# Performance work log

Hardware: AMD Instinct MI355X
Metric: run time of the kernel (lower is better)

Reference implementation:

```python
import jax, jax.numpy as jnp
import numpy as np

N_NODES = 50000
N_EDGES = 1600000
IN_C, HID_C, OUT_C = 1433, 128, 47


def setup_inputs() -> dict:
    key = jax.random.key(0)
    ks = jax.random.split(key, 5)
    x = jax.random.normal(ks[0], (N_NODES, IN_C), dtype=jnp.float32)
    edge_index = jax.random.randint(ks[1], (2, N_EDGES), 0, N_NODES, dtype=jnp.int32)
    # Glorot-ish init scaled by fan-in
    W1 = jax.random.normal(ks[2], (IN_C, HID_C), dtype=jnp.float32) / np.sqrt(IN_C)
    W2 = jax.random.normal(ks[3], (HID_C, HID_C), dtype=jnp.float32) / np.sqrt(HID_C)
    W3 = jax.random.normal(ks[4], (HID_C, OUT_C), dtype=jnp.float32) / np.sqrt(HID_C)
    b1 = jnp.zeros((HID_C,), jnp.float32)
    b2 = jnp.zeros((HID_C,), jnp.float32)
    b3 = jnp.zeros((OUT_C,), jnp.float32)
    return {"x": x, "edge_index": edge_index, "W1": W1, "b1": b1,
            "W2": W2, "b2": b2, "W3": W3, "b3": b3}


def _gcn_norm(edge_index, n_nodes, dtype):
    # PyG GCNConv default: add self-loops, symmetric D^-1/2 A D^-1/2 norm.
    loops = jnp.arange(n_nodes, dtype=edge_index.dtype)
    src = jnp.concatenate([edge_index[0], loops])
    dst = jnp.concatenate([edge_index[1], loops])
    deg = jax.ops.segment_sum(jnp.ones(src.shape[0], dtype), dst, num_segments=n_nodes)
    dinv = jax.lax.rsqrt(jnp.maximum(deg, 1.0))  # deg >= 1 due to self-loops
    norm = dinv[src] * dinv[dst]  # [E + N]
    return src, dst, norm


def _gcn_layer(h, W, b, src, dst, norm, n_nodes):
    hw = h @ W                       # [N, C_out] dense transform first (cheaper)
    msg = hw[src] * norm[:, None]    # gather + per-edge scale
    out = jax.ops.segment_sum(msg, dst, num_segments=n_nodes)  # scatter-add
    return out + b


def reference(x, edge_index, W1, b1, W2, b2, W3, b3):
    n = x.shape[0]
    src, dst, norm = _gcn_norm(edge_index, n, x.dtype)
    h = jax.nn.relu(_gcn_layer(x, W1, b1, src, dst, norm, n))
    # dropout is identity in eval mode (training=False)
    h = jax.nn.relu(_gcn_layer(h, W2, b2, src, dst, norm, n))
    return _gcn_layer(h, W3, b3, src, dst, norm, n)
```

## Files before the change

kernel.cpp:

```cpp
#include <hip/hip_runtime.h>
#include <math.h>
#include <stdint.h>

#define N_NODES 50000
#define N_EDGES 1600000
#define IN_C    1433
#define HID_C   128
#define OUT_C   47
#define KPAD1   1440

typedef unsigned short u16;

__device__ inline u16 f2bf(float x, float& hf) {
    unsigned u = __float_as_uint(x);
    unsigned r = (u + 0x7FFFu + ((u >> 16) & 1u)) & 0xFFFF0000u;
    hf = __uint_as_float(r);
    return (u16)(r >> 16);
}

__device__ inline void gld_lds16(const void* g, const void* lds) {
    __builtin_amdgcn_global_load_lds(
        (const __attribute__((address_space(1))) unsigned int*)(unsigned long long)(uintptr_t)g,
        (__attribute__((address_space(3))) unsigned int*)(unsigned long long)(unsigned)(uintptr_t)lds,
        16, 0, 0);
}

__global__ __launch_bounds__(256) void k_zero_i(int* p, int n) {
    int i = blockIdx.x * 256 + threadIdx.x;
    if (i < n) p[i] = 0;
}

__global__ __launch_bounds__(256) void k_count(const int* __restrict__ dst, int* __restrict__ cnt) {
    int e = blockIdx.x * 256 + threadIdx.x;
    if (e < N_EDGES) atomicAdd(&cnt[dst[e]], 1);
}

__global__ __launch_bounds__(256) void k_dinv(const int* __restrict__ cnt, float* __restrict__ dinv) {
    int i = blockIdx.x * 256 + threadIdx.x;
    if (i < N_NODES) dinv[i] = rsqrtf(1.0f + (float)cnt[i]);
}

__global__ __launch_bounds__(1024) void k_scan(const int* __restrict__ cnt, int* __restrict__ row_start) {
    __shared__ int sums[1024];
    const int t = threadIdx.x;
    const int CH = (N_NODES + 1023) / 1024;
    const int base = t * CH;
    int s = 0;
    for (int j = 0; j < CH; ++j) { int idx = base + j; if (idx < N_NODES) s += cnt[idx]; }
    sums[t] = s;
    __syncthreads();
    for (int off = 1; off < 1024; off <<= 1) {
        int v = (t >= off) ? sums[t - off] : 0;
        __syncthreads();
        sums[t] += v;
        __syncthreads();
    }
    int run = (t == 0) ? 0 : sums[t - 1];
    for (int j = 0; j < CH; ++j) {
        int idx = base + j;
        if (idx < N_NODES) { row_start[idx] = run; run += cnt[idx]; }
    }
    if (t == 1023) row_start[N_NODES] = N_EDGES;
}

__global__ __launch_bounds__(256) void k_fill(
    const int* __restrict__ src, const int* __restrict__ dst,
    const int* __restrict__ row_start, int* __restrict__ cursor,
    int* __restrict__ csr_src)
{
    int e = blockIdx.x * 256 + threadIdx.x;
    if (e >= N_EDGES) return;
    int t = dst[e];
    int pos = row_start[t] + atomicAdd(&cursor[t], 1);
    csr_src[pos] = src[e];
}

__global__ __launch_bounds__(256) void k_wsplit(
    const float* __restrict__ W, int K, int Kpad,
    u16* __restrict__ Thi, u16* __restrict__ Tlo)
{
    int id = blockIdx.x * 256 + threadIdx.x;
    if (id >= 128 * Kpad) return;
    int n = id / Kpad, k = id - n * Kpad;
    float v = (k < K) ? W[(long)k * HID_C + n] : 0.f;
    float hf; u16 h = f2bf(v, hf);
    float d;  u16 l = f2bf(v - hf, d);
    Thi[id] = h; Tlo[id] = l;
}

template<bool RELU_A>
__global__ __launch_bounds__(256) void k_gemm_mfma(
    const float* __restrict__ A, const u16* __restrict__ BThi,
    const u16* __restrict__ BTlo, float* __restrict__ C,
    int M, int K, int Kpad, int lda)
{
    using bf16x8 = __attribute__((ext_vector_type(8))) short;
    using f32x4  = __attribute__((ext_vector_type(4))) float;

    __shared__ float Af[2][2048];
    __shared__ u16  Bhs[2][4096];
    __shared__ u16  Bls[2][4096];

    const int tid  = threadIdx.x;
    const int wave = tid >> 6, lane = tid & 63;
    const int lr   = lane & 15, quad = lane >> 4;
    const int wm   = (wave >> 1) * 32, wn = (wave & 1) * 64;
    const int m0   = blockIdx.x * 64;

    f32x4 acc[2][4];
#pragma unroll
    for (int i = 0; i < 2; ++i)
#pragma unroll
        for (int j = 0; j < 4; ++j)
#pragma unroll
            for (int r = 0; r < 4; ++r) acc[i][j][r] = 0.f;

    const int nk = (K + 31) >> 5;

    auto stageB = [&](int t, int buf) {
        const int k0 = t * 32;
#pragma unroll
        for (int i = 0; i < 2; ++i) {
            const int gc  = wave * 128 + i * 64;
            const int g   = gc + lane;
            const int row = g >> 2, c = g & 3;
            const int q   = c ^ ((row >> 1) & 3);
            const long goff = (long)row * Kpad + k0 + q * 8;
            gld_lds16(BThi + goff, &Bhs[buf][gc * 8]);
            gld_lds16(BTlo + goff, &Bls[buf][gc * 8]);
        }
    };
    auto stageA = [&](int t, int buf) {
        const int k0 = t * 32;
        if (k0 + 32 <= K) {
#pragma unroll
            for (int i = 0; i < 2; ++i) {
                const int gc  = wave * 128 + i * 64;
                const int g   = gc + lane;
                const int row = g >> 3, c = g & 7;
                const int q   = c ^ (row & 7);
                int gm = m0 + row; if (gm >= M) gm = M - 1;
                gld_lds16(A + (long)gm * lda + k0 + q * 4, &Af[buf][gc * 4]);
            }
        } else {
#pragma unroll
            for (int i = 0; i < 2; ++i) {
                const int g   = wave * 128 + i * 64 + lane;
                const int row = g >> 3, c = g & 7;
                const int q   = c ^ (row & 7);
                int gm = m0 + row; if (gm >= M) gm = M - 1;
                const float* p = A + (long)gm * lda;
                const int kb = k0 + q * 4;
                float4 v;
                v.x = (kb + 0 < K) ? p[kb + 0] : 0.f;
                v.y = (kb + 1 < K) ? p[kb + 1] : 0.f;
                v.z = (kb + 2 < K) ? p[kb + 2] : 0.f;
                v.w = (kb + 3 < K) ? p[kb + 3] : 0.f;
                *(float4*)&Af[buf][g * 4] = v;
            }
        }
    };

    stageA(0, 0); stageB(0, 0);
    __syncthreads();

    for (int t = 0; t < nk; ++t) {
        const int buf = t & 1;
        if (t + 1 < nk) { stageA(t + 1, buf ^ 1); stageB(t + 1, buf ^ 1); }

        bf16x8 ah[2], al[2];
#pragma unroll
        for (int i = 0; i < 2; ++i) {
            const int row = wm + i * 16 + lr;
            const int rx  = row & 7;
            f32x4 x0 = *(const f32x4*)&Af[buf][row * 32 + (((2 * quad)     ^ rx) * 4)];
            f32x4 x1 = *(const f32x4*)&Af[buf][row * 32 + (((2 * quad + 1) ^ rx) * 4)];
            float a8[8] = {x0[0], x0[1], x0[2], x0[3], x1[0], x1[1], x1[2], x1[3]};
#pragma unroll
            for (int c = 0; c < 8; ++c) {
                float x = RELU_A ? fmaxf(a8[c], 0.f) : a8[c];
                float hf; u16 h = f2bf(x, hf);
                float d;  u16 l = f2bf(x - hf, d);
                ah[i][c] = (short)h; al[i][c] = (short)l;
            }
        }
        bf16x8 bh[4], bl[4];
#pragma unroll
        for (int j = 0; j < 4; ++j) {
            const int row = wn + j * 16 + lr;
            const int cs  = quad ^ ((row >> 1) & 3);
            bh[j] = *(const bf16x8*)&Bhs[buf][row * 32 + cs * 8];
            bl[j] = *(const bf16x8*)&Bls[buf][row * 32 + cs * 8];
        }
#pragma unroll
        for (int i = 0; i < 2; ++i)
#pragma unroll
            for (int j = 0; j < 4; ++j) {
                acc[i][j] = __builtin_amdgcn_mfma_f32_16x16x32_bf16(ah[i], bh[j], acc[i][j], 0, 0, 0);
                acc[i][j] = __builtin_amdgcn_mfma_f32_16x16x32_bf16(ah[i], bl[j], acc[i][j], 0, 0, 0);
                acc[i][j] = __builtin_amdgcn_mfma_f32_16x16x32_bf16(al[i], bh[j], acc[i][j], 0, 0, 0);
            }
        __syncthreads();
    }

#pragma unroll
    for (int i = 0; i < 2; ++i)
#pragma unroll
        for (int r = 0; r < 4; ++r) {
            int row = m0 + wm + i * 16 + quad * 4 + r;
            if (row < M) {
#pragma unroll
                for (int j = 0; j < 4; ++j)
                    C[(long)row * HID_C + wn + j * 16 + lr] = acc[i][j][r];
            }
        }
}

template<int BN, bool RELU_A, bool BIAS>
__global__ __launch_bounds__(256) void k_gemm(
    const float* __restrict__ A, const float* __restrict__ B,
    const float* __restrict__ bias, float* __restrict__ C,
    int M, int N, int K, int lda, int ldb, int ldc)
{
    constexpr int BM = 64, BK = 16;
    constexpr int TNV = BN / 64;
    __shared__ float As[BK][BM + 4];
    __shared__ float Bs[BK][BN];

    const int tid = threadIdx.x;
    const int tm = tid >> 4;
    const int tn = tid & 15;
    const int m0 = blockIdx.x * BM;
    const int n0 = blockIdx.y * BN;

    float acc[4][TNV * 4];
#pragma unroll
    for (int r = 0; r < 4; ++r)
#pragma unroll
        for (int c = 0; c < TNV * 4; ++c) acc[r][c] = 0.f;

    for (int k0 = 0; k0 < K; k0 += BK) {
        {
            int kk = tid & 15;
            int r0 = tid >> 4;
#pragma unroll
            for (int it = 0; it < 4; ++it) {
                int r = r0 + 16 * it;
                int gm = m0 + r, gk = k0 + kk;
                float v = 0.f;
                if (gm < M && gk < K) v = A[(long)gm * lda + gk];
                if (RELU_A) v = fmaxf(v, 0.f);
                As[kk][r] = v;
            }
        }
        {
            constexpr int KPP = 256 / BN;
            int n  = tid % BN;
            int kb = tid / BN;
#pragma unroll
            for (int it = 0; it < BK / KPP; ++it) {
                int kk = kb + KPP * it;
                int gk = k0 + kk, gn = n0 + n;
                float v = 0.f;
                if (gk < K && gn < N) v = B[(long)gk * ldb + gn];
                Bs[kk][n] = v;
            }
        }
        __syncthreads();
#pragma unroll
        for (int kk = 0; kk < BK; ++kk) {
            float4 a = *(const float4*)&As[kk][tm * 4];
            float av[4] = {a.x, a.y, a.z, a.w};
#pragma unroll
            for (int j = 0; j < TNV; ++j) {
                float4 b = *(const float4*)&Bs[kk][tn * 4 + 64 * j];
                float bv[4] = {b.x, b.y, b.z, b.w};
#pragma unroll
                for (int r = 0; r < 4; ++r)
#pragma unroll
                    for (int c = 0; c < 4; ++c)
                        acc[r][c + j * 4] += av[r] * bv[c];
            }
        }
        __syncthreads();
    }
#pragma unroll
    for (int r = 0; r < 4; ++r) {
        int gm = m0 + tm * 4 + r;
        if (gm >= M) continue;
#pragma unroll
        for (int j = 0; j < TNV; ++j)
#pragma unroll
            for (int c = 0; c < 4; ++c) {
                int gn = n0 + tn * 4 + 64 * j + c;
                if (gn < N) {
                    float v = acc[r][c + j * 4];
                    if (BIAS) v += bias[gn];
                    C[(long)gm * ldc + gn] = v;
                }
            }
    }
}

template<bool RELU_IN, bool BIAS>
__global__ __launch_bounds__(256) void k_aggregate(
    const float2* __restrict__ hw, const int* __restrict__ row_start,
    const int* __restrict__ csr_src, const float* __restrict__ dinv,
    const float* __restrict__ bias, float2* __restrict__ out)
{
    const int tid = threadIdx.x;
    const int node = blockIdx.x * 4 + (tid >> 6);
    if (node >= N_NODES) return;
    const int lane = tid & 63;

    float dt = dinv[node];
    float2 v = hw[(long)node * 64 + lane];
    if (RELU_IN) { v.x = fmaxf(v.x, 0.f); v.y = fmaxf(v.y, 0.f); }
    float2 acc = {0.f, 0.f};

    const int e1 = row_start[node + 1];
    int e = row_start[node];
    for (; e + 2 <= e1; e += 2) {
        int s0 = csr_src[e], s1 = csr_src[e + 1];
        float w0 = dinv[s0], w1 = dinv[s1];
        float2 u0 = hw[(long)s0 * 64 + lane];
        float2 u1 = hw[(long)s1 * 64 + lane];
        if (RELU_IN) {
            u0.x = fmaxf(u0.x, 0.f); u0.y = fmaxf(u0.y, 0.f);
            u1.x = fmaxf(u1.x, 0.f); u1.y = fmaxf(u1.y, 0.f);
        }
        acc.x += w0 * u0.x + w1 * u1.x;
        acc.y += w0 * u0.y + w1 * u1.y;
    }
    if (e < e1) {
        int s0 = csr_src[e];
        float w0 = dinv[s0];
        float2 u0 = hw[(long)s0 * 64 + lane];
        if (RELU_IN) { u0.x = fmaxf(u0.x, 0.f); u0.y = fmaxf(u0.y, 0.f); }
        acc.x += w0 * u0.x;
        acc.y += w0 * u0.y;
    }

    float2 r;
    r.x = dt * (acc.x + dt * v.x);
    r.y = dt * (acc.y + dt * v.y);
    if (BIAS) {
        float2 b = ((const float2*)bias)[lane];
        r.x += b.x; r.y += b.y;
    }
    out[(long)node * 64 + lane] = r;
}

__global__ __launch_bounds__(256) void k_aggregate47(
    const float* __restrict__ hw, const int* __restrict__ row_start,
    const int* __restrict__ csr_src, const float* __restrict__ dinv,
    const float* __restrict__ bias, float* __restrict__ out)
{
    const int tid = threadIdx.x;
    const int node = blockIdx.x * 4 + (tid >> 6);
    if (node >= N_NODES) return;
    const int lane = tid & 63;
    if (lane >= OUT_C) return;

    float dt = dinv[node];
    float v = hw[(long)node * 48 + lane];
    float acc = 0.f;

    const int e1 = row_start[node + 1];
    int e = row_start[node];
    for (; e + 2 <= e1; e += 2) {
        int s0 = csr_src[e], s1 = csr_src[e + 1];
        float w0 = dinv[s0], w1 = dinv[s1];
        float u0 = hw[(long)s0 * 48 + lane];
        float u1 = hw[(long)s1 * 48 + lane];
        acc += w0 * u0 + w1 * u1;
    }
    if (e < e1) {
        int s0 = csr_src[e];
        acc += dinv[s0] * hw[(long)s0 * 48 + lane];
    }

    out[(long)node * OUT_C + lane] = dt * (acc + dt * v) + bias[lane];
}

extern "C" void kernel_launch(void* const* d_in, const int* in_sizes, int n_in,
                              void* d_out, int out_size, void* d_ws, size_t ws_size,
                              hipStream_t stream) {
    const float* x  = (const float*)d_in[0];
    const int*   ei = (const int*)  d_in[1];
    const float* W1 = (const float*)d_in[2];
    const float* b1 = (const float*)d_in[3];
    const float* W2 = (const float*)d_in[4];
    const float* b2 = (const float*)d_in[5];
    const float* W3 = (const float*)d_in[6];
    const float* b3 = (const float*)d_in[7];
    float* out = (float*)d_out;
    const int* src = ei;
    const int* dst = ei + N_EDGES;

    char* ws = (char*)d_ws;
    float* dinv      = (float*)(ws + 0);
    int*   cnt       = (int*)  (ws + 200192);
    int*   cursor    = (int*)  (ws + 400384);
    int*   row_start = (int*)  (ws + 600576);
    int*   csr_src   = (int*)  (ws + 801280);
    float* bufA      = (float*)(ws + 7201280);
    float* bufB      = (float*)(ws + 32801280);
    u16*   W1Thi     = (u16*)  (ws + 58401280);
    u16*   W1Tlo     = (u16*)  (ws + 58769920);
    u16*   W2Thi     = (u16*)  (ws + 59138560);
    u16*   W2Tlo     = (u16*)  (ws + 59171328);

    dim3 blk(256);
    const int gN  = (N_NODES + 255) / 256;
    const int gE  = (N_EDGES + 255) / 256;
    const int gAg = (N_NODES + 3) / 4;
    const int gMf = (N_NODES + 63) / 64;
    dim3 gGemm((N_NODES + 63) / 64, 1);

    k_zero_i<<<gN, blk, 0, stream>>>(cnt, N_NODES);
    k_zero_i<<<gN, blk, 0, stream>>>(cursor, N_NODES);
    k_count<<<gE, blk, 0, stream>>>(dst, cnt);
    k_dinv<<<gN, blk, 0, stream>>>(cnt, dinv);
    k_scan<<<1, 1024, 0, stream>>>(cnt, row_start);
    k_fill<<<gE, blk, 0, stream>>>(src, dst, row_start, cursor, csr_src);

    k_wsplit<<<(128 * KPAD1 + 255) / 256, blk, 0, stream>>>(W1, IN_C, KPAD1, W1Thi, W1Tlo);
    k_wsplit<<<(128 * HID_C + 255) / 256, blk, 0, stream>>>(W2, HID_C, HID_C, W2Thi, W2Tlo);

    k_gemm_mfma<false><<<gMf, blk, 0, stream>>>(x, W1Thi, W1Tlo, bufA, N_NODES, IN_C, KPAD1, IN_C);
    k_aggregate<false, true><<<gAg, blk, 0, stream>>>(
        (const float2*)bufA, row_start, csr_src, dinv, b1, (float2*)bufB);

    k_gemm_mfma<true><<<gMf, blk, 0, stream>>>(bufB, W2Thi, W2Tlo, bufA, N_NODES, HID_C, HID_C, HID_C);
    k_aggregate<false, true><<<gAg, blk, 0, stream>>>(
        (const float2*)bufA, row_start, csr_src, dinv, b2, (float2*)bufB);

    k_gemm<64, true, false><<<gGemm, blk, 0, stream>>>(
        bufB, W3, nullptr, bufA, N_NODES, OUT_C, HID_C, HID_C, OUT_C, 48);
    k_aggregate47<<<gAg, blk, 0, stream>>>(
        bufA, row_start, csr_src, dinv, b3, out);
}
```

Before: 745.6 us.

## Load A operand directly to registers and triple-buffer B with manual vmcnt waits

The MFMA GEMM no longer stages the fp32 A tile through LDS. Each lane now loads its own 8-element K slices of two rows straight into registers, double-buffered across iterations. B hi/lo tiles move to a three-slot LDS ring with explicit s_waitcnt vmcnt counts and raw s_barrier calls, replacing __syncthreads. This aims to cut LDS traffic and barrier stalls and to deepen prefetch, but it relies on hand-counted outstanding loads being correct. The per-lane scalar A loads may also coalesce worse than the previous 16-byte LDS-direct loads.

```diff
diff --git a/kernel.cpp b/kernel.cpp
--- a/kernel.cpp
+++ b/kernel.cpp
@@ -23,6 +23,12 @@
         (const __attribute__((address_space(1))) unsigned int*)(unsigned long long)(uintptr_t)g,
         (__attribute__((address_space(3))) unsigned int*)(unsigned long long)(unsigned)(uintptr_t)lds,
         16, 0, 0);
+}
+
+__device__ inline void wg_barrier() {
+    asm volatile("" ::: "memory");
+    __builtin_amdgcn_s_barrier();
+    asm volatile("" ::: "memory");
 }
 
 __global__ __launch_bounds__(256) void k_zero_i(int* p, int n) {
@@ -97,15 +103,20 @@
     using bf16x8 = __attribute__((ext_vector_type(8))) short;
     using f32x4  = __attribute__((ext_vector_type(4))) float;
 
-    __shared__ float Af[2][2048];
-    __shared__ u16  Bhs[2][4096];
-    __shared__ u16  Bls[2][4096];
+    __shared__ u16 Bhs[3][4096];
+    __shared__ u16 Bls[3][4096];
 
     const int tid  = threadIdx.x;
     const int wave = tid >> 6, lane = tid & 63;
     const int lr   = lane & 15, quad = lane >> 4;
     const int wm   = (wave >> 1) * 32, wn = (wave & 1) * 64;
     const int m0   = blockIdx.x * 64;
+    const int kq   = quad * 8;
+
+    int rr0 = m0 + wm + lr;      if (rr0 >= M) rr0 = M - 1;
+    int rr1 = m0 + wm + 16 + lr; if (rr1 >= M) rr1 = M - 1;
+    const float* a0 = A + (long)rr0 * lda;
+    const float* a1 = A + (long)rr1 * lda;
 
     f32x4 acc[2][4];
 #pragma unroll
@@ -130,55 +141,30 @@
             gld_lds16(BTlo + goff, &Bls[buf][gc * 8]);
         }
     };
-    auto stageA = [&](int t, int buf) {
-        const int k0 = t * 32;
-        if (k0 + 32 <= K) {
-#pragma unroll
-            for (int i = 0; i < 2; ++i) {
-                const int gc  = wave * 128 + i * 64;
-                const int g   = gc + lane;
-                const int row = g >> 3, c = g & 7;
-                const int q   = c ^ (row & 7);
-                int gm = m0 + row; if (gm >= M) gm = M - 1;
-                gld_lds16(A + (long)gm * lda + k0 + q * 4, &Af[buf][gc * 4]);
-            }
+
+    auto loadA = [&](int t, float (&v)[16]) {
+        const int k0 = t * 32 + kq;
+        if (t * 32 + 32 <= K) {
+#pragma unroll
+            for (int i = 0; i < 8; ++i) { v[i] = a0[k0 + i]; v[8 + i] = a1[k0 + i]; }
         } else {
 #pragma unroll
-            for (int i = 0; i < 2; ++i) {
-                const int g   = wave * 128 + i * 64 + lane;
-                const int row = g >> 3, c = g & 7;
-                const int q   = c ^ (row & 7);
-                int gm = m0 + row; if (gm >= M) gm = M - 1;
-                const float* p = A + (long)gm * lda;
-                const int kb = k0 + q * 4;
-                float4 v;
-                v.x = (kb + 0 < K) ? p[kb + 0] : 0.f;
-                v.y = (kb + 1 < K) ? p[kb + 1] : 0.f;
-                v.z = (kb + 2 < K) ? p[kb + 2] : 0.f;
-                v.w = (kb + 3 < K) ? p[kb + 3] : 0.f;
-                *(float4*)&Af[buf][g * 4] = v;
+            for (int i = 0; i < 8; ++i) {
+                const int gk = k0 + i;
+                v[i]     = (gk < K) ? a0[gk] : 0.f;
+                v[8 + i] = (gk < K) ? a1[gk] : 0.f;
             }
         }
     };
 
-    stageA(0, 0); stageB(0, 0);
-    __syncthreads();
-
-    for (int t = 0; t < nk; ++t) {
-        const int buf = t & 1;
-        if (t + 1 < nk) { stageA(t + 1, buf ^ 1); stageB(t + 1, buf ^ 1); }
-
+    auto compute = [&](int buf, float (&cur)[16]) {
         bf16x8 ah[2], al[2];
 #pragma unroll
         for (int i = 0; i < 2; ++i) {
-            const int row = wm + i * 16 + lr;
-            const int rx  = row & 7;
-            f32x4 x0 = *(const f32x4*)&Af[buf][row * 32 + (((2 * quad)     ^ rx) * 4)];
-            f32x4 x1 = *(const f32x4*)&Af[buf][row * 32 + (((2 * quad + 1) ^ rx) * 4)];
-            float a8[8] = {x0[0], x0[1], x0[2], x0[3], x1[0], x1[1], x1[2], x1[3]};
 #pragma unroll
             for (int c = 0; c < 8; ++c) {
-                float x = RELU_A ? fmaxf(a8[c], 0.f) : a8[c];
+                float x = cur[i * 8 + c];
+                if (RELU_A) x = fmaxf(x, 0.f);
                 float hf; u16 h = f2bf(x, hf);
                 float d;  u16 l = f2bf(x - hf, d);
                 ah[i][c] = (short)h; al[i][c] = (short)l;
@@ -200,8 +186,42 @@
                 acc[i][j] = __builtin_amdgcn_mfma_f32_16x16x32_bf16(ah[i], bl[j], acc[i][j], 0, 0, 0);
                 acc[i][j] = __builtin_amdgcn_mfma_f32_16x16x32_bf16(al[i], bh[j], acc[i][j], 0, 0, 0);
             }
-        __syncthreads();
-    }
+    };
+
+    float vA0[16], vA1[16];
+
+    stageB(0, 0);
+    loadA(0, vA0);
+    if (nk > 1) stageB(1, 1);
+
+#define GEMM_WAIT(s)                                                        \
+    do {                                                                    \
+        if ((s) + 2 < nk)      asm volatile("s_waitcnt vmcnt(24)" ::: "memory"); \
+        else if ((s) + 1 < nk) asm volatile("s_waitcnt vmcnt(20)" ::: "memory"); \
+        else                   asm volatile("s_waitcnt vmcnt(0)"  ::: "memory"); \
+    } while (0)
+
+    int t = 0;
+    for (; t + 1 < nk; t += 2) {
+        loadA(t + 1, vA1);
+        if (t + 2 < nk) stageB(t + 2, (t + 2) % 3);
+        GEMM_WAIT(t);
+        wg_barrier();
+        compute(t % 3, vA0);
+        wg_barrier();
+        if (t + 2 < nk) loadA(t + 2, vA0);
+        if (t + 3 < nk) stageB(t + 3, (t + 3) % 3);
+        GEMM_WAIT(t + 1);
+        wg_barrier();
+        compute((t + 1) % 3, vA1);
+        wg_barrier();
+    }
+    if (t < nk) {
+        GEMM_WAIT(t);
+        wg_barrier();
+        compute(t % 3, vA0);
+    }
+#undef GEMM_WAIT
 
 #pragma unroll
     for (int i = 0; i < 2; ++i)
```

After: 776.3 us. +4.1%, slower.
